# Optimization experiments

Hardware: AMD Instinct MI355X
Metric: run time of the kernel (lower is better)

The kernel has to match this reference:

```python
import jax, jax.numpy as jnp
import numpy as np

# ---- constants (match init_kwargs / input_specs) ----
B, NPG, EPG = 512, 50, 60          # graphs, nodes/graph, edges/graph
D, V = 128, 100000                 # embedding_dim, num_items
SPLITS, SCALE = 4, 12.0            # euler steps, logit scale
N, E = B * NPG, B * EPG
STDV = 1.0 / np.sqrt(D)


def _seg_sum(vals, idx, n):
    return jax.ops.segment_sum(vals, idx, num_segments=n)


def _l2norm(x, eps=1e-12):
    return x / jnp.maximum(jnp.linalg.norm(x, axis=-1, keepdims=True), eps)


def setup_inputs() -> dict:
    key = jax.random.key(0)
    ks = jax.random.split(key, 40)
    u = lambda i, shape: jax.random.uniform(ks[i], shape, minval=-STDV, maxval=STDV, dtype=jnp.float32)
    offs = jnp.repeat(jnp.arange(B, dtype=jnp.int32) * NPG, EPG)
    inp = dict(
        iid=jax.random.randint(ks[0], (N,), 0, V),
        src=jax.random.randint(ks[1], (E,), 0, NPG).astype(jnp.int32) + offs,
        dst=jax.random.randint(ks[2], (E,), 0, NPG).astype(jnp.int32) + offs,
        edge_w=jax.random.uniform(ks[3], (E,), minval=0.1, maxval=1.0, dtype=jnp.float32),
        edge_t=jax.random.uniform(ks[4], (E,), dtype=jnp.float32),
        node_t=jax.random.uniform(ks[5], (N,), dtype=jnp.float32),
        emb=u(6, (V, D)),
        # GGNN layer (num_layers=1): W1, W2 and torch-layout GRUCell(2D -> D)
        W1=u(7, (D, D)), W2=u(8, (D, D)),
        gw_ih=u(9, (3 * D, 2 * D)), gw_hh=u(10, (3 * D, D)),
        gb_ih=u(11, (3 * D,)), gb_hh=u(12, (3 * D,)),
        # GraphGRUODE GCNConv weights (x@W + b), norm='both'
        Wxr=u(13, (D, D)), bxr=u(14, (D,)), Wxz=u(15, (D, D)), bxz=u(16, (D,)),
        Wxh=u(17, (D, D)), bxh=u(18, (D,)), Whr=u(19, (D, D)), bhr=u(20, (D,)),
        Whz=u(21, (D, D)), bhz=u(22, (D,)), Whh=u(23, (D, D)), bhh=u(24, (D,)),
        # AttnReadout
        Wu=u(25, (D, D)), Wv=u(26, (D, D)), bv=u(27, (D,)), We=u(28, (D, 1)),
        # fc_sr: [2D -> D], no bias
        W_sr=u(29, (2 * D, D)),
    )
    return inp


def reference(iid, src, dst, edge_w, edge_t, node_t, emb,
              W1, W2, gw_ih, gw_hh, gb_ih, gb_hh,
              Wxr, bxr, Wxz, bxz, Wxh, bxh, Whr, bhr, Whz, bhz, Whh, bhh,
              Wu, Wv, bv, We, W_sr):
    # ---- embedding + normalize ----
    feat = _l2norm(emb[iid])                                   # [N, D]

    # ---- GGNNLayer: weighted mean over in-edges, both directions, GRU cell ----
    wcol = edge_w[:, None]
    num1 = _seg_sum(feat[src] * wcol, dst, N)
    den1 = _seg_sum(edge_w, dst, N)
    neigh1 = num1 / jnp.where(den1 == 0, 1.0, den1)[:, None]    # zero for isolated nodes
    num2 = _seg_sum(feat[dst] * wcol, src, N)
    den2 = _seg_sum(edge_w, src, N)
    neigh2 = num2 / jnp.where(den2 == 0, 1.0, den2)[:, None]
    hn = jnp.concatenate([neigh1 @ W1, neigh2 @ W2], axis=1)    # [N, 2D]
    gi = hn @ gw_ih.T + gb_ih
    gh = feat @ gw_hh.T + gb_hh
    ir, iz, ig = jnp.split(gi, 3, axis=1)
    hr, hz, hg = jnp.split(gh, 3, axis=1)
    r = jax.nn.sigmoid(ir + hr)
    z = jax.nn.sigmoid(iz + hz)
    g = jnp.tanh(ig + r * hg)
    feat = (1.0 - z) * g + z * feat
    feat = _l2norm(feat)

    # ---- GraphGRUODE: euler integration over dynamic masked subgraphs ----
    x = feat
    t_end = edge_t.max()
    dt = t_end / SPLITS
    nodiag = src != dst

    def ode_f(t, h):
        nm = node_t >= t                                        # node subgraph mask
        em = (edge_t <= t) & nm[src] & nm[dst] & nodiag          # edge mask (no self-loops)
        emf = em.astype(h.dtype)
        deg = _seg_sum(emf, src, N) + _seg_sum(emf, dst, N)      # undirected degree (reverse edges added)
        dis = jnp.clip(deg, 1.0, None) ** -0.5

        def conv(inp, W, b):                                     # GCNConv, norm='both'
            s = inp * dis[:, None]
            agg = (_seg_sum(s[src] * emf[:, None], dst, N)
                   + _seg_sum(s[dst] * emf[:, None], src, N))
            return (agg * dis[:, None]) @ W + b

        rr = jax.nn.sigmoid(conv(x, Wxr, bxr) + conv(h, Whr, bhr))
        zz = jax.nn.sigmoid(conv(x, Wxz, bxz) + conv(h, Whz, bhz))
        uu = jnp.tanh(conv(x, Wxh, bxh) + conv(rr * h, Whh, bhh))
        dh = (1.0 - zz) * (uu - h)
        return jnp.where(nm[:, None], dh, 0.0)

    h = x
    for k in range(SPLITS):
        h = h + dt * ode_f(k * dt, h)
    feat = _l2norm(h)

    # ---- AttnReadout (fixed NPG nodes/graph -> reshape as segment ops) ----
    fb = feat.reshape(B, NPG, D)
    last = fb[:, -1, :]                                          # last node of each session
    e = jax.nn.sigmoid(fb @ Wu + (last @ Wv + bv)[:, None, :]) @ We   # [B, NPG, 1]
    alpha = jax.nn.softmax(e, axis=1)
    sr_g = jnp.sum(fb * alpha, axis=1)                           # [B, D]

    sr = _l2norm(jnp.concatenate([last, sr_g], axis=1) @ W_sr)   # [B, D]
    target = _l2norm(emb)                                        # [V, D]
    logits = sr @ target.T                                       # [B, V]
    return jax.nn.log_softmax(SCALE * logits, axis=-1)
```

## Files before the change

### kernel.cpp

```cpp
#include <hip/hip_runtime.h>

#define BB 512
#define NPG 50
#define EPG 60
#define DD 128
#define VV 100000
#define VPAD 100032
#define NSPLITS 4
#define FSCALE 12.0f
#define NN (BB*NPG)
#define EE (BB*EPG)
#define NDTOT (NN*DD)
#define NCB (VPAD/64)

typedef __attribute__((ext_vector_type(8))) short bfx8;
typedef __attribute__((ext_vector_type(4))) float f32x4;

__device__ __forceinline__ float sigmoidf_(float x){ return 1.f/(1.f+expf(-x)); }
__device__ __forceinline__ short f2bf(float f){
  union { float f; unsigned u; } v; v.f = f;
  unsigned r = v.u + 0x7FFF + ((v.u >> 16) & 1);
  return (short)(r >> 16);
}

__global__ __launch_bounds__(256) void k_embn(const float* __restrict__ emb, short* __restrict__ embn) {
  int row = blockIdx.x*4 + (threadIdx.x >> 6);
  int lane = threadIdx.x & 63;
  if (row >= VPAD) return;
  if (row >= VV) { embn[(size_t)row*DD+lane]=0; embn[(size_t)row*DD+64+lane]=0; return; }
  const float* r = emb + (size_t)row*DD;
  float a = r[lane], b = r[lane+64];
  float s = a*a + b*b;
  for (int off=32; off; off>>=1) s += __shfl_down(s, off);
  s = __shfl(s, 0);
  float inv = 1.0f/fmaxf(sqrtf(s), 1e-12f);
  embn[(size_t)row*DD+lane]    = f2bf(a*inv);
  embn[(size_t)row*DD+64+lane] = f2bf(b*inv);
}

__global__ __launch_bounds__(128) void k_gather(const int* __restrict__ iid, const float* __restrict__ emb,
                                                float* __restrict__ x, short* __restrict__ xb) {
  int n = blockIdx.x, d = threadIdx.x;
  int v = iid[n];
  float e = emb[(size_t)v*DD + d];
  __shared__ float red2[2];
  float ss = e*e;
  for (int off=32; off; off>>=1) ss += __shfl_down(ss, off);
  if ((d & 63)==0) red2[d>>6] = ss;
  __syncthreads();
  float inv = 1.f/fmaxf(sqrtf(red2[0]+red2[1]), 1e-12f);
  float f = e*inv;
  x[(size_t)n*DD + d] = f;
  xb[(size_t)n*DD + d] = f2bf(f);
}

__global__ __launch_bounds__(256) void k_dt(const float* __restrict__ edge_t, float* __restrict__ dtp) {
  __shared__ float red[256];
  float m = -1e30f;
  for (int e = threadIdx.x; e < EE; e += 256) m = fmaxf(m, edge_t[e]);
  red[threadIdx.x] = m; __syncthreads();
  for (int s=128; s; s>>=1){ if ((int)threadIdx.x < s) red[threadIdx.x] = fmaxf(red[threadIdx.x], red[threadIdx.x+s]); __syncthreads(); }
  if (threadIdx.x==0) dtp[0] = red[0] / (float)NSPLITS;
}

__global__ void k_m12t(const float* __restrict__ W1, const float* __restrict__ W2,
                       const float* __restrict__ gw_ih, short* __restrict__ M12t) {
  int c = blockIdx.x, k = threadIdx.x;
  const float* Wrow = (k < 128) ? (W1 + (size_t)k*128) : (W2 + (size_t)(k-128)*128);
  const float* grow = gw_ih + (size_t)c*256 + ((k < 128) ? 0 : 128);
  float s = 0.f;
  for (int j = 0; j < 128; ++j) s += Wrow[j]*grow[j];
  M12t[(size_t)c*256 + k] = f2bf(s);
}
__global__ void k_bfcopy(const float* __restrict__ src, short* __restrict__ dst) {
  size_t i = (size_t)blockIdx.x*blockDim.x + threadIdx.x;
  dst[i] = f2bf(src[i]);
}
__global__ void k_wrzt(const float* __restrict__ Wxr, const float* __restrict__ Wxz,
                       const float* __restrict__ Whr, const float* __restrict__ Whz,
                       short* __restrict__ Wrzt) {
  int c = blockIdx.x, k = threadIdx.x;
  float v;
  if (k < 128) v = (c < 128) ? Wxr[k*128+c] : Wxz[k*128+(c-128)];
  else         v = (c < 128) ? Whr[(k-128)*128+c] : Whz[(k-128)*128+(c-128)];
  Wrzt[(size_t)c*256 + k] = f2bf(v);
}
__global__ void k_wu2t(const float* __restrict__ Wxh, const float* __restrict__ Whh, short* __restrict__ Wu2t) {
  int c = blockIdx.x, k = threadIdx.x;
  float v = (k < 128) ? Wxh[k*128+c] : Whh[(k-128)*128+c];
  Wu2t[(size_t)c*256 + k] = f2bf(v);
}
__global__ void k_wt128(const float* __restrict__ W, short* __restrict__ Wt) {
  int c = blockIdx.x, k = threadIdx.x;
  Wt[(size_t)c*128 + k] = f2bf(W[(size_t)k*128 + c]);
}
__global__ void k_build_bias(const float* __restrict__ bxr, const float* __restrict__ bhr,
                             const float* __restrict__ bxz, const float* __restrict__ bhz,
                             const float* __restrict__ bxh, const float* __restrict__ bhh,
                             float* __restrict__ brz, float* __restrict__ bu) {
  int t = threadIdx.x;
  if (t < 128) brz[t] = bxr[t] + bhr[t];
  else if (t < 256) brz[t] = bxz[t-128] + bhz[t-128];
  else bu[t-256] = bxh[t-256] + bhh[t-256];
}

__global__ __launch_bounds__(256) void k_grp_mean(const int* __restrict__ src, const int* __restrict__ dst,
                                                  const float* __restrict__ ew, const float* __restrict__ feat,
                                                  short* __restrict__ ABb) {
  __shared__ float fl[NPG*128];
  __shared__ float n1[NPG*128];
  __shared__ float n2[NPG*128];
  __shared__ int sl[EPG], tl[EPG];
  __shared__ float wl[EPG];
  __shared__ float d1[NPG], d2[NPG];
  int b = blockIdx.x, tid = threadIdx.x;
  int nb = b*NPG, eb = b*EPG;
  for (int i = tid; i < NPG*32; i += 256) {
    ((float4*)fl)[i] = ((const float4*)(feat + (size_t)nb*128))[i];
    ((float4*)n1)[i] = make_float4(0.f,0.f,0.f,0.f);
    ((float4*)n2)[i] = make_float4(0.f,0.f,0.f,0.f);
  }
  if (tid < EPG) { sl[tid] = src[eb+tid]-nb; tl[tid] = dst[eb+tid]-nb; wl[tid] = ew[eb+tid]; }
  __syncthreads();
  const int dgrp = tid >> 7, d = tid & 127;
  if (dgrp == 0) {
    for (int e = 0; e < EPG; ++e) n1[tl[e]*128+d] += fl[sl[e]*128+d]*wl[e];
  } else {
    for (int e = 0; e < EPG; ++e) n2[sl[e]*128+d] += fl[tl[e]*128+d]*wl[e];
  }
  if (tid < NPG) {
    float den = 0.f;
    for (int e = 0; e < EPG; ++e) den += (tl[e]==tid) ? wl[e] : 0.f;
    d1[tid] = (den == 0.f) ? 1.f : den;
  } else if (tid >= 128 && tid < 128+NPG) {
    int dd = tid - 128;
    float den = 0.f;
    for (int e = 0; e < EPG; ++e) den += (sl[e]==dd) ? wl[e] : 0.f;
    d2[dd] = (den == 0.f) ? 1.f : den;
  }
  __syncthreads();
  for (int n = 0; n < NPG; ++n) {
    float v = dgrp ? (n2[n*128+d]/d2[n]) : (n1[n*128+d]/d1[n]);
    ABb[(size_t)(nb+n)*256 + dgrp*128 + d] = f2bf(v);
  }
}

__global__ __launch_bounds__(128) void k_gru(const float* __restrict__ gi, const float* __restrict__ gh,
                                             float* __restrict__ x) {
  int n = blockIdx.x, d = threadIdx.x;
  const float* gin = gi + (size_t)n*384;
  const float* ghn = gh + (size_t)n*384;
  float ir = gin[d], iz = gin[128+d], ig = gin[256+d];
  float hr = ghn[d], hz = ghn[128+d], hg = ghn[256+d];
  float f0 = x[(size_t)n*DD + d];
  float r = sigmoidf_(ir + hr);
  float z = sigmoidf_(iz + hz);
  float g = tanhf(ig + r*hg);
  float f = (1.f - z)*g + z*f0;
  __shared__ float red2[2];
  float ss = f*f;
  for (int off=32; off; off>>=1) ss += __shfl_down(ss, off);
  if ((d & 63)==0) red2[d>>6] = ss;
  __syncthreads();
  float inv = 1.f/fmaxf(sqrtf(red2[0]+red2[1]), 1e-12f);
  x[(size_t)n*DD + d] = f*inv;
}

__global__ __launch_bounds__(256) void k_ode_fused(
    const int* __restrict__ src, const int* __restrict__ dst,
    const float* __restrict__ edge_t, const float* __restrict__ node_t,
    const float* __restrict__ dtp,
    float* __restrict__ x, short* __restrict__ fbb,
    const short* __restrict__ Wrzt, const short* __restrict__ Wu2t,
    const float* __restrict__ brz, const float* __restrict__ bu)
{
  __shared__ __align__(16) float xl[NPG*128];
  __shared__ __align__(16) float hl[NPG*128];
  __shared__ __align__(16) float S1[NPG*128];
  __shared__ __align__(16) float S2[NPG*128];
  __shared__ __align__(16) float zzl[NPG*128];
  __shared__ __align__(16) short aggX[64*136];
  __shared__ __align__(16) short aggH[64*136];
  __shared__ int stl[EPG];
  __shared__ float etl[EPG];
  __shared__ float ntl[NPG];
  __shared__ float disl[NPG];
  __shared__ unsigned long long actm_s;
  __shared__ float red4[4];

  const int b = blockIdx.x, tid = threadIdx.x;
  const int nb = b*NPG, eb = b*EPG;
  const int wave = tid>>6, lane = tid&63, quad = lane>>4, l16 = lane&15;
  const float dtv = dtp[0];

  for (int i = tid; i < NPG*32; i += 256) {
    float4 v = ((const float4*)(x + (size_t)nb*128))[i];
    ((float4*)xl)[i] = v;
    ((float4*)hl)[i] = v;
  }
  if (tid < EPG) { stl[tid] = (src[eb+tid]-nb) | ((dst[eb+tid]-nb)<<16); etl[tid] = edge_t[eb+tid]; }
  if (tid >= 64 && tid < 64+NPG) ntl[tid-64] = node_t[nb+tid-64];
  for (int i = tid; i < 14*136; i += 256) { aggX[50*136 + i] = 0; aggH[50*136 + i] = 0; }
  __syncthreads();

  for (int ks = 0; ks < NSPLITS; ++ks) {
    const float t = (float)ks * dtv;
    if (wave == 0) {
      bool p = false;
      if (lane < EPG) {
        int st = stl[lane]; int s = st & 0xffff, tt = st >> 16;
        p = (etl[lane] <= t) && (ntl[s] >= t) && (ntl[tt] >= t) && (s != tt);
      }
      unsigned long long m = __ballot(p);
      if (lane == 0) actm_s = m;
    }
    for (int i = tid; i < NPG*128; i += 256) { S1[i] = 0.f; S2[i] = 0.f; }
    __syncthreads();
    const unsigned long long actm = actm_s;
    if (tid < NPG) {
      float deg = 0.f;
      for (int e = 0; e < EPG; ++e) {
        if ((actm >> e) & 1ULL) {
          int st = stl[e]; int s = st & 0xffff, tt = st >> 16;
          deg += (s==tid ? 1.f:0.f) + (tt==tid ? 1.f:0.f);
        }
      }
      disl[tid] = rsqrtf(fmaxf(deg, 1.f));
    }
    __syncthreads();
    if (tid < 128) {
      const int d = tid;
      for (int e = 0; e < EPG; ++e) {
        if ((actm >> e) & 1ULL) {
          int st = stl[e]; int s = st & 0xffff, tt = st >> 16;
          float ds_ = disl[s], dt_ = disl[tt];
          S1[tt*128+d] += xl[s*128+d]*ds_;
          S1[s*128+d]  += xl[tt*128+d]*dt_;
          S2[tt*128+d] += hl[s*128+d]*ds_;
          S2[s*128+d]  += hl[tt*128+d]*dt_;
        }
      }
    }
    __syncthreads();
    for (int i = tid; i < NPG*128; i += 256) {
      int r = i >> 7, c = i & 127;
      aggX[r*136 + c] = f2bf(S1[i]*disl[r]);
      aggH[r*136 + c] = f2bf(S2[i]*disl[r]);
    }
    __syncthreads();
    {
      f32x4 acc[4][4] = {{{0.f,0.f,0.f,0.f},{0.f,0.f,0.f,0.f},{0.f,0.f,0.f,0.f},{0.f,0.f,0.f,0.f}},
                         {{0.f,0.f,0.f,0.f},{0.f,0.f,0.f,0.f},{0.f,0.f,0.f,0.f},{0.f,0.f,0.f,0.f}},
                         {{0.f,0.f,0.f,0.f},{0.f,0.f,0.f,0.f},{0.f,0.f,0.f,0.f},{0.f,0.f,0.f,0.f}},
                         {{0.f,0.f,0.f,0.f},{0.f,0.f,0.f,0.f},{0.f,0.f,0.f,0.f},{0.f,0.f,0.f,0.f}}};
      for (int k0 = 0; k0 < 256; k0 += 32) {
        const short* Ab = (k0 < 128) ? aggX : aggH;
        const int kk = (k0 & 127) + quad*8;
        bfx8 af[4];
#pragma unroll
        for (int m = 0; m < 4; ++m) af[m] = *(const bfx8*)&Ab[(m*16+l16)*136 + kk];
#pragma unroll
        for (int n = 0; n < 4; ++n) {
          const int bn = (wave*4+n)*16 + l16;
          bfx8 bf = *(const bfx8*)&Wrzt[(size_t)bn*256 + k0 + quad*8];
#pragma unroll
          for (int m = 0; m < 4; ++m)
            acc[m][n] = __builtin_amdgcn_mfma_f32_16x16x32_bf16(af[m], bf, acc[m][n], 0, 0, 0);
        }
      }
#pragma unroll
      for (int n = 0; n < 4; ++n) {
        const int col = (wave*4+n)*16 + l16;
        const float bb = brz[col];
#pragma unroll
        for (int m = 0; m < 4; ++m)
#pragma unroll
          for (int r = 0; r < 4; ++r) {
            const int row = m*16 + quad*4 + r;
            if (row < NPG) {
              float s = sigmoidf_(acc[m][n][r] + bb);
              if (col < 128) S1[row*128+col] = s * hl[row*128+col];
              else           zzl[row*128+col-128] = s;
            }
          }
      }
    }
    __syncthreads();
    for (int i = tid; i < NPG*128; i += 256) S2[i] = 0.f;
    __syncthreads();
    if (tid < 128) {
      const int d = tid;
      for (int e = 0; e < EPG; ++e) {
        if ((actm >> e) & 1ULL) {
          int st = stl[e]; int s = st & 0xffff, tt = st >> 16;
          S2[tt*128+d] += S1[s*128+d]*disl[s];
          S2[s*128+d]  += S1[tt*128+d]*disl[tt];
        }
      }
    }
    __syncthreads();
    for (int i = tid; i < NPG*128; i += 256) {
      int r = i >> 7, c = i & 127;
      aggH[r*136 + c] = f2bf(S2[i]*disl[r]);
    }
    __syncthreads();
    {
      f32x4 acc[4][2] = {{{0.f,0.f,0.f,0.f},{0.f,0.f,0.f,0.f}},
                         {{0.f,0.f,0.f,0.f},{0.f,0.f,0.f,0.f}},
                         {{0.f,0.f,0.f,0.f},{0.f,0.f,0.f,0.f}},
                         {{0.f,0.f,0.f,0.f},{0.f,0.f,0.f,0.f}}};
      for (int k0 = 0; k0 < 256; k0 += 32) {
        const short* Ab = (k0 < 128) ? aggX : aggH;
        const int kk = (k0 & 127) + quad*8;
        bfx8 af[4];
#pragma unroll
        for (int m = 0; m < 4; ++m) af[m] = *(const bfx8*)&Ab[(m*16+l16)*136 + kk];
#pragma unroll
        for (int n = 0; n < 2; ++n) {
          const int bn = (wave*2+n)*16 + l16;
          bfx8 bf = *(const bfx8*)&Wu2t[(size_t)bn*256 + k0 + quad*8];
#pragma unroll
          for (int m = 0; m < 4; ++m)
            acc[m][n] = __builtin_amdgcn_mfma_f32_16x16x32_bf16(af[m], bf, acc[m][n], 0, 0, 0);
        }
      }
#pragma unroll
      for (int n = 0; n < 2; ++n) {
        const int col = (wave*2+n)*16 + l16;
        const float bb = bu[col];
#pragma unroll
        for (int m = 0; m < 4; ++m)
#pragma unroll
          for (int r = 0; r < 4; ++r) {
            const int row = m*16 + quad*4 + r;
            if (row < NPG && ntl[row] >= t) {
              float hv = hl[row*128+col];
              float uu = tanhf(acc[m][n][r] + bb);
              float zv = zzl[row*128+col];
              hl[row*128+col] = hv + dtv*(1.f - zv)*(uu - hv);
            }
          }
      }
    }
    __syncthreads();
  }

  for (int rp = 0; rp < NPG; rp += 2) {
    const int r = rp + (tid>>7);
    const int d = tid & 127;
    float v = hl[r*128 + d];
    float ss = v*v;
    for (int off=32; off; off>>=1) ss += __shfl_down(ss, off);
    if (lane == 0) red4[wave] = ss;
    __syncthreads();
    int w0 = (tid>>7)*2;
    float inv = 1.f/fmaxf(sqrtf(red4[w0]+red4[w0+1]), 1e-12f);
    float f = v*inv;
    x[(size_t)(nb+r)*128 + d] = f;
    fbb[(size_t)(nb+r)*128 + d] = f2bf(f);
    __syncthreads();
  }
}

__global__ __launch_bounds__(256) void gemm_mfma(
    const short* __restrict__ A, int lda,
    const short* __restrict__ Bt, int ldbt,
    const float* __restrict__ bias,
    float* __restrict__ C, int ldc,
    int K, int mode,
    float* __restrict__ outp, float* __restrict__ pmax, float* __restrict__ psum)
{
  __shared__ short As[64*40];
  __shared__ short Bs[64*40];
  const int tid = threadIdx.x;
  const int wave = tid >> 6, lane = tid & 63;
  const int wr = wave >> 1, wc = wave & 1;
  const int quad = lane >> 4, l16 = lane & 15;
  int rb, cb;
  if (mode >= 4) {
    int t = (blockIdx.x & 7)*1563 + (blockIdx.x >> 3);
    rb = t & 7; cb = t >> 3;
  } else { rb = blockIdx.y; cb = blockIdx.x; }
  const int row0 = rb*64, col0 = cb*64;
  f32x4 acc[2][2] = {{{0.f,0.f,0.f,0.f},{0.f,0.f,0.f,0.f}},{{0.f,0.f,0.f,0.f},{0.f,0.f,0.f,0.f}}};
  const int sm = tid >> 2, skq = tid & 3;
  const short* Ap = A + (size_t)(row0+sm)*lda + skq*8;
  const short* Bp = Bt + (size_t)(col0+sm)*ldbt + skq*8;
  for (int k0 = 0; k0 < K; k0 += 32) {
    *(bfx8*)&As[sm*40 + skq*8] = *(const bfx8*)(Ap + k0);
    *(bfx8*)&Bs[sm*40 + skq*8] = *(const bfx8*)(Bp + k0);
    __syncthreads();
    bfx8 a0 = *(bfx8*)&As[(wr*32 + l16)*40 + quad*8];
    bfx8 a1 = *(bfx8*)&As[(wr*32 + 16 + l16)*40 + quad*8];
    bfx8 b0 = *(bfx8*)&Bs[(wc*32 + l16)*40 + quad*8];
    bfx8 b1 = *(bfx8*)&Bs[(wc*32 + 16 + l16)*40 + quad*8];
    acc[0][0] = __builtin_amdgcn_mfma_f32_16x16x32_bf16(a0, b0, acc[0][0], 0, 0, 0);
    acc[0][1] = __builtin_amdgcn_mfma_f32_16x16x32_bf16(a0, b1, acc[0][1], 0, 0, 0);
    acc[1][0] = __builtin_amdgcn_mfma_f32_16x16x32_bf16(a1, b0, acc[1][0], 0, 0, 0);
    acc[1][1] = __builtin_amdgcn_mfma_f32_16x16x32_bf16(a1, b1, acc[1][1], 0, 0, 0);
    __syncthreads();
  }

  if (mode == 0) {
#pragma unroll
    for (int i = 0; i < 2; ++i)
#pragma unroll
      for (int j = 0; j < 2; ++j) {
        int gc = col0 + wc*32 + j*16 + l16;
        float bb = bias ? bias[gc] : 0.f;
#pragma unroll
        for (int r = 0; r < 4; ++r) {
          int gr = row0 + wr*32 + i*16 + quad*4 + r;
          C[(size_t)gr*ldc + gc] = acc[i][j][r] + bb;
        }
      }
  } else if (mode == 4) {
    __shared__ float pm[64][2], ps[64][2];
    int c0 = col0 + wc*32 + l16;
    int c1 = c0 + 16;
#pragma unroll
    for (int i = 0; i < 2; ++i) {
#pragma unroll
      for (int r = 0; r < 4; ++r) {
        int rloc = wr*32 + i*16 + quad*4 + r;
        float v0 = (c0 < VV) ? acc[i][0][r] : -1e30f;
        float v1 = (c1 < VV) ? acc[i][1][r] : -1e30f;
        float m = fmaxf(v0, v1);
#pragma unroll
        for (int off = 1; off < 16; off <<= 1) m = fmaxf(m, __shfl_xor(m, off));
        float s = expf(v0 - m) + expf(v1 - m);
#pragma unroll
        for (int off = 1; off < 16; off <<= 1) s += __shfl_xor(s, off);
        if (l16 == 0) { pm[rloc][wc] = m; ps[rloc][wc] = s; }
      }
    }
    __syncthreads();
    if (tid < 64) {
      float m0 = pm[tid][0], m1 = pm[tid][1];
      float s0 = ps[tid][0], s1 = ps[tid][1];
      float M = fmaxf(m0, m1);
      float S = s0*expf(m0 - M) + s1*expf(m1 - M);
      pmax[(size_t)(row0 + tid)*NCB + cb] = M;
      psum[(size_t)(row0 + tid)*NCB + cb] = S;
    }
  } else {
#pragma unroll
    for (int i = 0; i < 2; ++i) {
#pragma unroll
      for (int r = 0; r < 4; ++r) {
        int gr = row0 + wr*32 + i*16 + quad*4 + r;
        float l = bias[gr];
#pragma unroll
        for (int j = 0; j < 2; ++j) {
          int gc = col0 + wc*32 + j*16 + l16;
          if (gc < VV) outp[(size_t)gr*VV + gc] = acc[i][j][r] - l;
        }
      }
    }
  }
}

__global__ __launch_bounds__(128) void k_attn(const float* __restrict__ fb, const float* __restrict__ U,
                                              const float* __restrict__ lv, const float* __restrict__ We,
                                              const float* __restrict__ W_sr, short* __restrict__ srvb) {
  int b = blockIdx.x, d = threadIdx.x;
  __shared__ float sc[NPG];
  __shared__ float lastv[DD], srg[DD];
  __shared__ float red2[2];
  const float* Ub  = U  + (size_t)b*NPG*DD;
  const float* lvb = lv + (size_t)b*DD;
  if (d < 64) {
    for (int i=0;i<NPG;++i) {
      float e = We[d]   * sigmoidf_(Ub[i*DD + d]      + lvb[d]) +
                We[d+64]* sigmoidf_(Ub[i*DD + 64 + d] + lvb[d+64]);
      for (int off=32; off; off>>=1) e += __shfl_down(e, off);
      if (d==0) sc[i] = e;
    }
  }
  __syncthreads();
  if (d < 64) {
    float v = (d < NPG) ? sc[d] : -1e30f;
    float m = v;
    for (int off=1; off<64; off<<=1) m = fmaxf(m, __shfl_xor(m, off));
    float ex = (d < NPG) ? expf(v - m) : 0.f;
    float s = ex;
    for (int off=1; off<64; off<<=1) s += __shfl_xor(s, off);
    if (d < NPG) sc[d] = ex/s;
  }
  __syncthreads();
  const float* fbb = fb + (size_t)b*NPG*DD;
  float lastd = fbb[(NPG-1)*DD + d];
  float sg = 0.f;
  for (int i=0;i<NPG;++i) sg += fbb[i*DD + d]*sc[i];
  lastv[d] = lastd; srg[d] = sg;
  __syncthreads();
  float acc = 0.f;
  for (int k=0;k<DD;++k) acc += lastv[k]*W_sr[k*DD + d];
  for (int k=0;k<DD;++k) acc += srg[k]*W_sr[(DD+k)*DD + d];
  float ss = acc*acc;
  for (int off=32; off; off>>=1) ss += __shfl_down(ss, off);
  if ((d & 63)==0) red2[d>>6] = ss;
  __syncthreads();
  float inv = 1.f/fmaxf(sqrtf(red2[0]+red2[1]), 1e-12f);
  srvb[(size_t)b*DD + d] = f2bf(FSCALE*acc*inv);
}

__global__ __launch_bounds__(256) void k_lse(const float* __restrict__ pmax, const float* __restrict__ psum,
                                             float* __restrict__ lse) {
  int r = blockIdx.x, tid = threadIdx.x;
  float m = -1e30f, s = 0.f;
  for (int cb = tid; cb < NCB; cb += 256) {
    float m2 = pmax[(size_t)r*NCB + cb], s2 = psum[(size_t)r*NCB + cb];
    float M = fmaxf(m, m2);
    s = s*expf(m - M) + s2*expf(m2 - M);
    m = M;
  }
  __shared__ float ms[256], ssh[256];
  ms[tid] = m; ssh[tid] = s; __syncthreads();
  for (int st=128; st; st>>=1) {
    if (tid < st) {
      float m2 = ms[tid+st], s2 = ssh[tid+st];
      float M = fmaxf(ms[tid], m2);
      ssh[tid] = ssh[tid]*expf(ms[tid]-M) + s2*expf(m2-M);
      ms[tid] = M;
    }
    __syncthreads();
  }
  if (tid==0) lse[r] = ms[0] + logf(ssh[0]);
}

extern "C" void kernel_launch(void* const* d_in, const int* in_sizes, int n_in,
                              void* d_out, int out_size, void* d_ws, size_t ws_size,
                              hipStream_t stream) {
  (void)in_sizes; (void)n_in; (void)out_size; (void)ws_size;
  const int*   iid    = (const int*)  d_in[0];
  const int*   src    = (const int*)  d_in[1];
  const int*   dst    = (const int*)  d_in[2];
  const float* edge_w = (const float*)d_in[3];
  const float* edge_t = (const float*)d_in[4];
  const float* node_t = (const float*)d_in[5];
  const float* emb    = (const float*)d_in[6];
  const float* W1     = (const float*)d_in[7];
  const float* W2     = (const float*)d_in[8];
  const float* gw_ih  = (const float*)d_in[9];
  const float* gw_hh  = (const float*)d_in[10];
  const float* gb_ih  = (const float*)d_in[11];
  const float* gb_hh  = (const float*)d_in[12];
  const float* Wxr = (const float*)d_in[13]; const float* bxr = (const float*)d_in[14];
  const float* Wxz = (const float*)d_in[15]; const float* bxz = (const float*)d_in[16];
  const float* Wxh = (const float*)d_in[17]; const float* bxh = (const float*)d_in[18];
  const float* Whr = (const float*)d_in[19]; const float* bhr = (const float*)d_in[20];
  const float* Whz = (const float*)d_in[21]; const float* bhz = (const float*)d_in[22];
  const float* Whh = (const float*)d_in[23]; const float* bhh = (const float*)d_in[24];
  const float* Wu  = (const float*)d_in[25];
  const float* Wv  = (const float*)d_in[26]; const float* bv  = (const float*)d_in[27];
  const float* We  = (const float*)d_in[28];
  const float* W_sr= (const float*)d_in[29];

  float* ws  = (float*)d_ws;
  float* out = (float*)d_out;

  short* embn = (short*)ws;
  float* pmax = ws + 6402048;
  float* psum = pmax + 800256;
  short* M12t = (short*)(psum + 800256);
  short* gwhhb= (short*)(psum + 800256 + 49152);
  short* Wrzt = (short*)(psum + 800256 + 73728);
  short* Wu2t = (short*)(psum + 800256 + 106496);
  short* Wut  = (short*)(psum + 800256 + 122880);
  short* Wvt  = (short*)(psum + 800256 + 131072);
  float* brz  = psum + 800256 + 139264;
  float* bu   = brz + 256;
  float* lv   = bu + 128;
  float* dtp  = lv + 65536;
  float* lse  = dtp + 4;
  short* srvb = (short*)(lse + 512);

  short* ABb = (short*)out;
  float* x   = out + (size_t) 4*1024*1024;
  float* gi  = out + (size_t)20*1024*1024;
  float* gh  = out + (size_t)30*1024*1024;
  float* U   = out + (size_t)20*1024*1024;
  short* xb  = (short*)(out + (size_t)40*1024*1024);
  short* fbb = (short*)(out + (size_t)42*1024*1024);

  k_embn<<<VPAD/4, 256, 0, stream>>>(emb, embn);
  k_gather<<<NN, 128, 0, stream>>>(iid, emb, x, xb);
  k_dt<<<1, 256, 0, stream>>>(edge_t, dtp);
  k_m12t<<<384, 256, 0, stream>>>(W1, W2, gw_ih, M12t);
  k_bfcopy<<<384, 128, 0, stream>>>(gw_hh, gwhhb);
  k_wrzt<<<256, 256, 0, stream>>>(Wxr, Wxz, Whr, Whz, Wrzt);
  k_wu2t<<<128, 256, 0, stream>>>(Wxh, Whh, Wu2t);
  k_wt128<<<128, 128, 0, stream>>>(Wu, Wut);
  k_wt128<<<128, 128, 0, stream>>>(Wv, Wvt);
  k_build_bias<<<1, 384, 0, stream>>>(bxr, bhr, bxz, bhz, bxh, bhh, brz, bu);

  k_grp_mean<<<BB, 256, 0, stream>>>(src, dst, edge_w, x, ABb);

  gemm_mfma<<<dim3(6,400), 256, 0, stream>>>(ABb, 256, M12t, 256, gb_ih, gi, 384, 256, 0,
      nullptr, nullptr, nullptr);
  gemm_mfma<<<dim3(6,400), 256, 0, stream>>>(xb, 128, gwhhb, 128, gb_hh, gh, 384, 128, 0,
      nullptr, nullptr, nullptr);
  k_gru<<<NN, 128, 0, stream>>>(gi, gh, x);

  k_ode_fused<<<BB, 256, 0, stream>>>(src, dst, edge_t, node_t, dtp, x, fbb, Wrzt, Wu2t, brz, bu);

  gemm_mfma<<<dim3(2,400), 256, 0, stream>>>(fbb, 128, Wut, 128, nullptr, U, 128, 128, 0,
      nullptr, nullptr, nullptr);
  gemm_mfma<<<dim3(2,8), 256, 0, stream>>>(fbb + (size_t)(NPG-1)*DD, NPG*DD, Wvt, 128, bv, lv, 128, 128, 0,
      nullptr, nullptr, nullptr);
  k_attn<<<BB, 128, 0, stream>>>(x, U, lv, We, W_sr, srvb);

  gemm_mfma<<<dim3(8*NCB), 256, 0, stream>>>(srvb, 128, embn, 128, nullptr, nullptr, 0, 128, 4,
      nullptr, pmax, psum);
  k_lse<<<BB, 256, 0, stream>>>(pmax, psum, lse);
  gemm_mfma<<<dim3(8*NCB), 256, 0, stream>>>(srvb, 128, embn, 128, lse, nullptr, 0, 128, 5,
      out, nullptr, nullptr);
}
```

Before: 813.5 us.

## Replace edge-scatter aggregation with per-node CSR gather in ODE and mean kernels

Builds a per-graph CSR adjacency in shared memory so each output element gathers its neighbours, instead of one 128-thread group serially scattering over all edges. The ODE kernel moves to 512 threads with 2 blocks per CU, cuts shared memory by dropping several float buffers (x read from global, z kept in registers, r*h stored as bf16), and splits the r/z GEMM across 8 waves. The aim is more parallelism and occupancy in the aggregation-bound kernels. The cost is extra CSR build passes and the reduced precision of the r*h term.

```diff
diff --git a/kernel.cpp b/kernel.cpp
--- a/kernel.cpp
+++ b/kernel.cpp
@@ -12,6 +12,7 @@
 #define EE (BB*EPG)
 #define NDTOT (NN*DD)
 #define NCB (VPAD/64)
+#define ASTR 140
 
 typedef __attribute__((ext_vector_type(8))) short bfx8;
 typedef __attribute__((ext_vector_type(4))) float f32x4;
@@ -21,6 +22,10 @@
   union { float f; unsigned u; } v; v.f = f;
   unsigned r = v.u + 0x7FFF + ((v.u >> 16) & 1);
   return (short)(r >> 16);
+}
+__device__ __forceinline__ float bf2f(short s){
+  union { unsigned u; float f; } v; v.u = ((unsigned)(unsigned short)s) << 16;
+  return v.f;
 }
 
 __global__ __launch_bounds__(256) void k_embn(const float* __restrict__ emb, short* __restrict__ embn) {
@@ -107,41 +112,54 @@
 __global__ __launch_bounds__(256) void k_grp_mean(const int* __restrict__ src, const int* __restrict__ dst,
                                                   const float* __restrict__ ew, const float* __restrict__ feat,
                                                   short* __restrict__ ABb) {
-  __shared__ float fl[NPG*128];
-  __shared__ float n1[NPG*128];
-  __shared__ float n2[NPG*128];
-  __shared__ int sl[EPG], tl[EPG];
+  __shared__ int stl[EPG];
   __shared__ float wl[EPG];
-  __shared__ float d1[NPG], d2[NPG];
+  __shared__ int rp1[NPG+1], rp2[NPG+1];
+  __shared__ short ci1[EPG], ci2[EPG];
+  __shared__ float den1[NPG], den2[NPG];
+  __shared__ int c1[NPG], c2[NPG];
   int b = blockIdx.x, tid = threadIdx.x;
   int nb = b*NPG, eb = b*EPG;
-  for (int i = tid; i < NPG*32; i += 256) {
-    ((float4*)fl)[i] = ((const float4*)(feat + (size_t)nb*128))[i];
-    ((float4*)n1)[i] = make_float4(0.f,0.f,0.f,0.f);
-    ((float4*)n2)[i] = make_float4(0.f,0.f,0.f,0.f);
-  }
-  if (tid < EPG) { sl[tid] = src[eb+tid]-nb; tl[tid] = dst[eb+tid]-nb; wl[tid] = ew[eb+tid]; }
-  __syncthreads();
-  const int dgrp = tid >> 7, d = tid & 127;
-  if (dgrp == 0) {
-    for (int e = 0; e < EPG; ++e) n1[tl[e]*128+d] += fl[sl[e]*128+d]*wl[e];
-  } else {
-    for (int e = 0; e < EPG; ++e) n2[sl[e]*128+d] += fl[tl[e]*128+d]*wl[e];
-  }
+  if (tid < EPG) { stl[tid] = (src[eb+tid]-nb) | ((dst[eb+tid]-nb)<<16); wl[tid] = ew[eb+tid]; }
+  __syncthreads();
   if (tid < NPG) {
-    float den = 0.f;
-    for (int e = 0; e < EPG; ++e) den += (tl[e]==tid) ? wl[e] : 0.f;
-    d1[tid] = (den == 0.f) ? 1.f : den;
-  } else if (tid >= 128 && tid < 128+NPG) {
-    int dd = tid - 128;
-    float den = 0.f;
-    for (int e = 0; e < EPG; ++e) den += (sl[e]==dd) ? wl[e] : 0.f;
-    d2[dd] = (den == 0.f) ? 1.f : den;
-  }
-  __syncthreads();
-  for (int n = 0; n < NPG; ++n) {
-    float v = dgrp ? (n2[n*128+d]/d2[n]) : (n1[n*128+d]/d1[n]);
-    ABb[(size_t)(nb+n)*256 + dgrp*128 + d] = f2bf(v);
+    int a = 0, bc = 0; float dA = 0.f, dB = 0.f;
+    for (int e = 0; e < EPG; ++e) {
+      int st = stl[e]; int s = st & 0xffff, t = st >> 16;
+      if (t == tid) { a++;  dA += wl[e]; }
+      if (s == tid) { bc++; dB += wl[e]; }
+    }
+    c1[tid] = a; c2[tid] = bc;
+    den1[tid] = (dA == 0.f) ? 1.f : dA;
+    den2[tid] = (dB == 0.f) ? 1.f : dB;
+  }
+  __syncthreads();
+  if (tid == 0) { int acc = 0; for (int n = 0; n < NPG; ++n) { rp1[n] = acc; acc += c1[n]; } rp1[NPG] = acc; }
+  if (tid == 1) { int acc = 0; for (int n = 0; n < NPG; ++n) { rp2[n] = acc; acc += c2[n]; } rp2[NPG] = acc; }
+  __syncthreads();
+  if (tid < NPG) {
+    int w1 = rp1[tid], w2 = rp2[tid];
+    for (int e = 0; e < EPG; ++e) {
+      int st = stl[e]; int s = st & 0xffff, t = st >> 16;
+      if (t == tid) ci1[w1++] = (short)(s | (e<<8));
+      if (s == tid) ci2[w2++] = (short)(t | (e<<8));
+    }
+  }
+  __syncthreads();
+  const float* fg = feat + (size_t)nb*128;
+  for (int i = tid; i < NPG*128; i += 256) {
+    int n = i >> 7, d = i & 127;
+    float a1 = 0.f, a2 = 0.f;
+    for (int idx = rp1[n]; idx < rp1[n+1]; ++idx) {
+      int v = ci1[idx]; int j = v & 255, e = v >> 8;
+      a1 += fg[j*128 + d] * wl[e];
+    }
+    for (int idx = rp2[n]; idx < rp2[n+1]; ++idx) {
+      int v = ci2[idx]; int j = v & 255, e = v >> 8;
+      a2 += fg[j*128 + d] * wl[e];
+    }
+    ABb[(size_t)(nb+n)*256 + d]       = f2bf(a1/den1[n]);
+    ABb[(size_t)(nb+n)*256 + 128 + d] = f2bf(a2/den2[n]);
   }
 }
 
@@ -166,7 +184,7 @@
   x[(size_t)n*DD + d] = f*inv;
 }
 
-__global__ __launch_bounds__(256) void k_ode_fused(
+__global__ __launch_bounds__(512, 2) void k_ode_fused(
     const int* __restrict__ src, const int* __restrict__ dst,
     const float* __restrict__ edge_t, const float* __restrict__ node_t,
     const float* __restrict__ dtp,
@@ -174,34 +192,55 @@
     const short* __restrict__ Wrzt, const short* __restrict__ Wu2t,
     const float* __restrict__ brz, const float* __restrict__ bu)
 {
-  __shared__ __align__(16) float xl[NPG*128];
   __shared__ __align__(16) float hl[NPG*128];
-  __shared__ __align__(16) float S1[NPG*128];
-  __shared__ __align__(16) float S2[NPG*128];
-  __shared__ __align__(16) float zzl[NPG*128];
-  __shared__ __align__(16) short aggX[64*136];
-  __shared__ __align__(16) short aggH[64*136];
-  __shared__ int stl[EPG];
+  __shared__ __align__(16) short rhb[NPG*ASTR];
+  __shared__ __align__(16) short aggX[64*ASTR];
+  __shared__ __align__(16) short aggH[64*ASTR];
+  __shared__ int   rp[NPG+1];
+  __shared__ short ci[2*EPG];
+  __shared__ int   cnt[NPG];
+  __shared__ int   stl[EPG];
   __shared__ float etl[EPG];
   __shared__ float ntl[NPG];
   __shared__ float disl[NPG];
   __shared__ unsigned long long actm_s;
-  __shared__ float red4[4];
+  __shared__ float red8[8];
 
   const int b = blockIdx.x, tid = threadIdx.x;
   const int nb = b*NPG, eb = b*EPG;
   const int wave = tid>>6, lane = tid&63, quad = lane>>4, l16 = lane&15;
   const float dtv = dtp[0];
-
-  for (int i = tid; i < NPG*32; i += 256) {
-    float4 v = ((const float4*)(x + (size_t)nb*128))[i];
-    ((float4*)xl)[i] = v;
-    ((float4*)hl)[i] = v;
-  }
+  const float* xg = x + (size_t)nb*128;
+
+  for (int i = tid; i < NPG*32; i += 512)
+    ((float4*)hl)[i] = ((const float4*)xg)[i];
   if (tid < EPG) { stl[tid] = (src[eb+tid]-nb) | ((dst[eb+tid]-nb)<<16); etl[tid] = edge_t[eb+tid]; }
   if (tid >= 64 && tid < 64+NPG) ntl[tid-64] = node_t[nb+tid-64];
-  for (int i = tid; i < 14*136; i += 256) { aggX[50*136 + i] = 0; aggH[50*136 + i] = 0; }
-  __syncthreads();
+  for (int i = tid; i < 14*ASTR; i += 512) { aggX[NPG*ASTR + i] = 0; aggH[NPG*ASTR + i] = 0; }
+  __syncthreads();
+
+  if (tid < NPG) {
+    int c = 0;
+    for (int e = 0; e < EPG; ++e) {
+      int st = stl[e]; int s = st & 0xffff, t = st >> 16;
+      c += (s==tid) + (t==tid);
+    }
+    cnt[tid] = c;
+  }
+  __syncthreads();
+  if (tid == 0) { int acc = 0; for (int n = 0; n < NPG; ++n) { rp[n] = acc; acc += cnt[n]; } rp[NPG] = acc; }
+  __syncthreads();
+  if (tid < NPG) {
+    int w = rp[tid];
+    for (int e = 0; e < EPG; ++e) {
+      int st = stl[e]; int s = st & 0xffff, t = st >> 16;
+      if (t == tid) ci[w++] = (short)(s | (e<<8));
+      if (s == tid) ci[w++] = (short)(t | (e<<8));
+    }
+  }
+  __syncthreads();
+
+  float zreg[4][2][4];
 
   for (int ks = 0; ks < NSPLITS; ++ks) {
     const float t = (float)ks * dtv;
@@ -213,97 +252,35 @@
       }
       unsigned long long m = __ballot(p);
       if (lane == 0) actm_s = m;
-    }
-    for (int i = tid; i < NPG*128; i += 256) { S1[i] = 0.f; S2[i] = 0.f; }
+      if (lane < NPG) {
+        float deg = 0.f;
+        for (int idx = rp[lane]; idx < rp[lane+1]; ++idx) {
+          int e = ((int)ci[idx]) >> 8;
+          deg += (float)((m >> e) & 1ULL);
+        }
+        disl[lane] = rsqrtf(fmaxf(deg, 1.f));
+      }
+    }
     __syncthreads();
     const unsigned long long actm = actm_s;
-    if (tid < NPG) {
-      float deg = 0.f;
-      for (int e = 0; e < EPG; ++e) {
+
+    for (int i = tid; i < NPG*128; i += 512) {
+      int n = i >> 7, d = i & 127;
+      float ax = 0.f, ah = 0.f;
+      for (int idx = rp[n]; idx < rp[n+1]; ++idx) {
+        int v = ci[idx]; int j = v & 255, e = v >> 8;
         if ((actm >> e) & 1ULL) {
-          int st = stl[e]; int s = st & 0xffff, tt = st >> 16;
-          deg += (s==tid ? 1.f:0.f) + (tt==tid ? 1.f:0.f);
+          float dj = disl[j];
+          ax += xg[j*128 + d] * dj;
+          ah += hl[j*128 + d] * dj;
         }
       }
-      disl[tid] = rsqrtf(fmaxf(deg, 1.f));
-    }
-    __syncthreads();
-    if (tid < 128) {
-      const int d = tid;
-      for (int e = 0; e < EPG; ++e) {
-        if ((actm >> e) & 1ULL) {
-          int st = stl[e]; int s = st & 0xffff, tt = st >> 16;
-          float ds_ = disl[s], dt_ = disl[tt];
-          S1[tt*128+d] += xl[s*128+d]*ds_;
-          S1[s*128+d]  += xl[tt*128+d]*dt_;
-          S2[tt*128+d] += hl[s*128+d]*ds_;
-          S2[s*128+d]  += hl[tt*128+d]*dt_;
-        }
-      }
-    }
-    __syncthreads();
-    for (int i = tid; i < NPG*128; i += 256) {
-      int r = i >> 7, c = i & 127;
-      aggX[r*136 + c] = f2bf(S1[i]*disl[r]);
-      aggH[r*136 + c] = f2bf(S2[i]*disl[r]);
-    }
-    __syncthreads();
-    {
-      f32x4 acc[4][4] = {{{0.f,0.f,0.f,0.f},{0.f,0.f,0.f,0.f},{0.f,0.f,0.f,0.f},{0.f,0.f,0.f,0.f}},
-                         {{0.f,0.f,0.f,0.f},{0.f,0.f,0.f,0.f},{0.f,0.f,0.f,0.f},{0.f,0.f,0.f,0.f}},
-                         {{0.f,0.f,0.f,0.f},{0.f,0.f,0.f,0.f},{0.f,0.f,0.f,0.f},{0.f,0.f,0.f,0.f}},
-                         {{0.f,0.f,0.f,0.f},{0.f,0.f,0.f,0.f},{0.f,0.f,0.f,0.f},{0.f,0.f,0.f,0.f}}};
-      for (int k0 = 0; k0 < 256; k0 += 32) {
-        const short* Ab = (k0 < 128) ? aggX : aggH;
-        const int kk = (k0 & 127) + quad*8;
-        bfx8 af[4];
-#pragma unroll
-        for (int m = 0; m < 4; ++m) af[m] = *(const bfx8*)&Ab[(m*16+l16)*136 + kk];
-#pragma unroll
-        for (int n = 0; n < 4; ++n) {
-          const int bn = (wave*4+n)*16 + l16;
-          bfx8 bf = *(const bfx8*)&Wrzt[(size_t)bn*256 + k0 + quad*8];
-#pragma unroll
-          for (int m = 0; m < 4; ++m)
-            acc[m][n] = __builtin_amdgcn_mfma_f32_16x16x32_bf16(af[m], bf, acc[m][n], 0, 0, 0);
-        }
-      }
-#pragma unroll
-      for (int n = 0; n < 4; ++n) {
-        const int col = (wave*4+n)*16 + l16;
-        const float bb = brz[col];
-#pragma unroll
-        for (int m = 0; m < 4; ++m)
-#pragma unroll
-          for (int r = 0; r < 4; ++r) {
-            const int row = m*16 + quad*4 + r;
-            if (row < NPG) {
-              float s = sigmoidf_(acc[m][n][r] + bb);
-              if (col < 128) S1[row*128+col] = s * hl[row*128+col];
-              else           zzl[row*128+col-128] = s;
-            }
-          }
-      }
-    }
-    __syncthreads();
-    for (int i = tid; i < NPG*128; i += 256) S2[i] = 0.f;
-    __syncthreads();
-    if (tid < 128) {
-      const int d = tid;
-      for (int e = 0; e < EPG; ++e) {
-        if ((actm >> e) & 1ULL) {
-          int st = stl[e]; int s = st & 0xffff, tt = st >> 16;
-          S2[tt*128+d] += S1[s*128+d]*disl[s];
-          S2[s*128+d]  += S1[tt*128+d]*disl[tt];
-        }
-      }
-    }
-    __syncthreads();
-    for (int i = tid; i < NPG*128; i += 256) {
-      int r = i >> 7, c = i & 127;
-      aggH[r*136 + c] = f2bf(S2[i]*disl[r]);
-    }
-    __syncthreads();
+      float dn = disl[n];
+      aggX[n*ASTR + d] = f2bf(ax*dn);
+      aggH[n*ASTR + d] = f2bf(ah*dn);
+    }
+    __syncthreads();
+
     {
       f32x4 acc[4][2] = {{{0.f,0.f,0.f,0.f},{0.f,0.f,0.f,0.f}},
                          {{0.f,0.f,0.f,0.f},{0.f,0.f,0.f,0.f}},
@@ -314,11 +291,11 @@
         const int kk = (k0 & 127) + quad*8;
         bfx8 af[4];
 #pragma unroll
-        for (int m = 0; m < 4; ++m) af[m] = *(const bfx8*)&Ab[(m*16+l16)*136 + kk];
+        for (int m = 0; m < 4; ++m) af[m] = *(const bfx8*)&Ab[(m*16+l16)*ASTR + kk];
 #pragma unroll
         for (int n = 0; n < 2; ++n) {
           const int bn = (wave*2+n)*16 + l16;
-          bfx8 bf = *(const bfx8*)&Wu2t[(size_t)bn*256 + k0 + quad*8];
+          bfx8 bf = *(const bfx8*)&Wrzt[(size_t)bn*256 + k0 + quad*8];
 #pragma unroll
           for (int m = 0; m < 4; ++m)
             acc[m][n] = __builtin_amdgcn_mfma_f32_16x16x32_bf16(af[m], bf, acc[m][n], 0, 0, 0);
@@ -327,17 +304,67 @@
 #pragma unroll
       for (int n = 0; n < 2; ++n) {
         const int col = (wave*2+n)*16 + l16;
-        const float bb = bu[col];
+        const float bb = brz[col];
+#pragma unroll
+        for (int m = 0; m < 4; ++m)
+#pragma unroll
+          for (int r = 0; r < 4; ++r) {
+            const int row = m*16 + quad*4 + r;
+            float s = sigmoidf_(acc[m][n][r] + bb);
+            if (wave < 4) {
+              if (row < NPG) rhb[row*ASTR + col] = f2bf(s * hl[row*128 + col]);
+            } else {
+              zreg[m][n][r] = s;
+            }
+          }
+      }
+    }
+    __syncthreads();
+
+    for (int i = tid; i < NPG*128; i += 512) {
+      int n = i >> 7, d = i & 127;
+      float ar = 0.f;
+      for (int idx = rp[n]; idx < rp[n+1]; ++idx) {
+        int v = ci[idx]; int j = v & 255, e = v >> 8;
+        if ((actm >> e) & 1ULL) ar += bf2f(rhb[j*ASTR + d]) * disl[j];
+      }
+      aggH[n*ASTR + d] = f2bf(ar*disl[n]);
+    }
+    __syncthreads();
+
+    if (wave >= 4) {
+      f32x4 acc2[4][2] = {{{0.f,0.f,0.f,0.f},{0.f,0.f,0.f,0.f}},
+                          {{0.f,0.f,0.f,0.f},{0.f,0.f,0.f,0.f}},
+                          {{0.f,0.f,0.f,0.f},{0.f,0.f,0.f,0.f}},
+                          {{0.f,0.f,0.f,0.f},{0.f,0.f,0.f,0.f}}};
+      for (int k0 = 0; k0 < 256; k0 += 32) {
+        const short* Ab = (k0 < 128) ? aggX : aggH;
+        const int kk = (k0 & 127) + quad*8;
+        bfx8 af[4];
+#pragma unroll
+        for (int m = 0; m < 4; ++m) af[m] = *(const bfx8*)&Ab[(m*16+l16)*ASTR + kk];
+#pragma unroll
+        for (int n = 0; n < 2; ++n) {
+          const int col2 = ((wave-4)*2+n)*16 + l16;
+          bfx8 bf = *(const bfx8*)&Wu2t[(size_t)col2*256 + k0 + quad*8];
+#pragma unroll
+          for (int m = 0; m < 4; ++m)
+            acc2[m][n] = __builtin_amdgcn_mfma_f32_16x16x32_bf16(af[m], bf, acc2[m][n], 0, 0, 0);
+        }
+      }
+#pragma unroll
+      for (int n = 0; n < 2; ++n) {
+        const int col2 = ((wave-4)*2+n)*16 + l16;
+        const float bb = bu[col2];
 #pragma unroll
         for (int m = 0; m < 4; ++m)
 #pragma unroll
           for (int r = 0; r < 4; ++r) {
             const int row = m*16 + quad*4 + r;
             if (row < NPG && ntl[row] >= t) {
-              float hv = hl[row*128+col];
-              float uu = tanhf(acc[m][n][r] + bb);
-              float zv = zzl[row*128+col];
-              hl[row*128+col] = hv + dtv*(1.f - zv)*(uu - hv);
+              float hv = hl[row*128 + col2];
+              float uu = tanhf(acc2[m][n][r] + bb);
+              hl[row*128 + col2] = hv + dtv*(1.f - zreg[m][n][r])*(uu - hv);
             }
           }
       }
@@ -345,19 +372,21 @@
     __syncthreads();
   }
 
-  for (int rp = 0; rp < NPG; rp += 2) {
-    const int r = rp + (tid>>7);
+  for (int rp_ = 0; rp_ < NPG; rp_ += 4) {
+    const int r = rp_ + (tid>>7);
     const int d = tid & 127;
-    float v = hl[r*128 + d];
+    float v = (r < NPG) ? hl[r*128 + d] : 0.f;
     float ss = v*v;
     for (int off=32; off; off>>=1) ss += __shfl_down(ss, off);
-    if (lane == 0) red4[wave] = ss;
-    __syncthreads();
-    int w0 = (tid>>7)*2;
-    float inv = 1.f/fmaxf(sqrtf(red4[w0]+red4[w0+1]), 1e-12f);
-    float f = v*inv;
-    x[(size_t)(nb+r)*128 + d] = f;
-    fbb[(size_t)(nb+r)*128 + d] = f2bf(f);
+    if (lane == 0) red8[wave] = ss;
+    __syncthreads();
+    int g = tid>>7;
+    float inv = 1.f/fmaxf(sqrtf(red8[2*g]+red8[2*g+1]), 1e-12f);
+    if (r < NPG) {
+      float f = v*inv;
+      x[(size_t)(nb+r)*128 + d] = f;
+      fbb[(size_t)(nb+r)*128 + d] = f2bf(f);
+    }
     __syncthreads();
   }
 }
@@ -603,7 +632,7 @@
       nullptr, nullptr, nullptr);
   k_gru<<<NN, 128, 0, stream>>>(gi, gh, x);
 
-  k_ode_fused<<<BB, 256, 0, stream>>>(src, dst, edge_t, node_t, dtp, x, fbb, Wrzt, Wu2t, brz, bu);
+  k_ode_fused<<<BB, 512, 0, stream>>>(src, dst, edge_t, node_t, dtp, x, fbb, Wrzt, Wu2t, brz, bu);
 
   gemm_mfma<<<dim3(2,400), 256, 0, stream>>>(fbb, 128, Wut, 128, nullptr, U, 128, 128, 0,
       nullptr, nullptr, nullptr);
```

Result: slower. 854.1 us (+5.0%).
